# Optimization experiments

Measured on AMD Instinct MI355X. Metric: run time of the kernel, lower is better.

The kernel has to match this reference:

```python
import jax, jax.numpy as jnp
import numpy as np

B, OUT_LEN, IN_LEN, H = 8, 1024, 4096, 256


def setup_inputs() -> dict:
    key = jax.random.key(0)
    k1, k2, k3 = jax.random.split(key, 3)
    output = jax.random.normal(k1, (B, OUT_LEN, H), dtype=jnp.float32)
    encoder_outputs = jax.random.normal(k2, (B, IN_LEN, H), dtype=jnp.float32)
    # valid lengths in [1, IN_LEN] so every softmax row has >=1 unmasked entry
    lengths = jax.random.randint(k3, (B,), 1, IN_LEN + 1).astype(jnp.int32)
    return {"output": output, "encoder_outputs": encoder_outputs, "lengths": lengths}


def reference(output, encoder_outputs, lengths):
    # scores: [B, out_len, in_len], unscaled dot-product (as in the original)
    scores = jnp.einsum('boh,bih->boi', output, encoder_outputs)
    # mask[b, j] = j < lengths[b]; masked positions get -inf (additive mask)
    valid = jnp.arange(encoder_outputs.shape[1])[None, :] < lengths[:, None]  # [B, in_len]
    scores = jnp.where(valid[:, None, :], scores, -jnp.inf)
    attn = jax.nn.softmax(scores, axis=-1)  # [B, out_len, in_len]
    context = jnp.einsum('boi,bih->boh', attn, encoder_outputs)  # [B, out_len, H]
    return (context, attn)
```

## Files before the change

### kernel.cpp

```cpp
#include <hip/hip_runtime.h>
#include <hip/hip_bf16.h>
#include <math.h>

#define B_    8
#define OLEN  1024
#define ILEN  4096
#define HDIM  256
#define LDA   40

typedef __attribute__((ext_vector_type(8))) short bf16x8;
typedef __attribute__((ext_vector_type(4))) float f32x4;

__device__ inline unsigned pk_bf16(float x, float y) {
  union { __hip_bfloat162 h; unsigned u; } c;
  c.h = __float22bfloat162_rn(make_float2(x, y));
  return c.u;
}
__device__ inline short f2bf(float x) {
  union { __hip_bfloat16 h; short s; } c;
  c.h = __float2bfloat16(x);
  return c.s;
}

struct HiLo { uint4 hi, lo; };
__device__ inline HiLo split8(const float* __restrict__ p) {
  float4 v0 = *(const float4*)p;
  float4 v1 = *(const float4*)(p + 4);
  float f[8] = {v0.x, v0.y, v0.z, v0.w, v1.x, v1.y, v1.z, v1.w};
  unsigned hu[8]; float lo[8];
#pragma unroll
  for (int i = 0; i < 8; ++i) {
    unsigned u = __float_as_uint(f[i]);
    hu[i] = u & 0xffff0000u;
    lo[i] = f[i] - __uint_as_float(hu[i]);
  }
  HiLo r;
  r.hi = make_uint4((hu[0] >> 16) | hu[1], (hu[2] >> 16) | hu[3],
                    (hu[4] >> 16) | hu[5], (hu[6] >> 16) | hu[7]);
  r.lo = make_uint4(pk_bf16(lo[0], lo[1]), pk_bf16(lo[2], lo[3]),
                    pk_bf16(lo[4], lo[5]), pk_bf16(lo[6], lo[7]));
  return r;
}

__device__ inline void gl_lds16(const void* g, void* l) {
  __builtin_amdgcn_global_load_lds(
      (const __attribute__((address_space(1))) unsigned*)g,
      (__attribute__((address_space(3))) unsigned*)(l), 16, 0, 0);
}

__global__ __launch_bounds__(256) void k_prep_q(const float* __restrict__ Q,
                                                short* __restrict__ Qhi,
                                                short* __restrict__ Qlo) {
  const size_t idx = ((size_t)blockIdx.x * 256 + threadIdx.x) * 8;
  HiLo r = split8(&Q[idx]);
  *(uint4*)&Qhi[idx] = r.hi;
  *(uint4*)&Qlo[idx] = r.lo;
}

__global__ __launch_bounds__(256) void k_prep_e(const float* __restrict__ E,
                                                short* __restrict__ Ehi,
                                                short* __restrict__ Elo,
                                                short* __restrict__ ET,
                                                const int* __restrict__ len) {
  const int it = blockIdx.x, ht = blockIdx.y, b = blockIdx.z;
  const int L = len[b];
  const int t = threadIdx.x;
  if (it * 32 >= L) {
    const int h = t >> 3, i0 = (t & 7) * 4;
    *(uint2*)&ET[((size_t)(b * HDIM + ht * 32 + h)) * ILEN + it * 32 + i0] =
        make_uint2(0u, 0u);
    return;
  }
  __shared__ short Lsh[32][36];
  {
    const int i = t >> 3, h0 = (t & 7) * 4;
    const size_t gidx = ((size_t)(b * ILEN + it * 32 + i)) * HDIM + ht * 32 + h0;
    float4 v = *(const float4*)&E[gidx];
    float f[4] = {v.x, v.y, v.z, v.w};
    unsigned hs[4]; float lo[4];
#pragma unroll
    for (int j = 0; j < 4; ++j) {
      unsigned u = __float_as_uint(f[j]);
      hs[j] = u & 0xffff0000u;
      lo[j] = f[j] - __uint_as_float(hs[j]);
    }
    *(uint2*)&Ehi[gidx] = make_uint2((hs[0] >> 16) | hs[1], (hs[2] >> 16) | hs[3]);
    *(uint2*)&Elo[gidx] = make_uint2(pk_bf16(lo[0], lo[1]), pk_bf16(lo[2], lo[3]));
    Lsh[h0 + 0][i] = f2bf(f[0]);
    Lsh[h0 + 1][i] = f2bf(f[1]);
    Lsh[h0 + 2][i] = f2bf(f[2]);
    Lsh[h0 + 3][i] = f2bf(f[3]);
  }
  __syncthreads();
  {
    const int h = t >> 3, i0 = (t & 7) * 4;
    *(uint2*)&ET[((size_t)(b * HDIM + ht * 32 + h)) * ILEN + it * 32 + i0] =
        *(const uint2*)&Lsh[h][i0];
  }
}

__global__ __launch_bounds__(256) void k_scores_pre(
    const short* __restrict__ Qhi, const short* __restrict__ Qlo,
    const short* __restrict__ Ehi, const short* __restrict__ Elo,
    float* __restrict__ S, float2* __restrict__ stat,
    const int* __restrict__ len) {
  const int it = blockIdx.x, ot = blockIdx.y, b = blockIdx.z;
  const int L = len[b];
  if (it * 128 >= L) return;

  const size_t qoff = ((size_t)b * OLEN + ot * 128) * HDIM;
  const size_t eoff = ((size_t)b * ILEN + it * 128) * HDIM;

  __shared__ __align__(16) short Ah[128 * 32], Al[128 * 32];
  __shared__ __align__(16) short Bh[128 * 32], Bl[128 * 32];

  const int t = threadIdx.x;
  const int w = t >> 6, l = t & 63;
  const int la = l & 15, quad = l >> 4;
  const int mw = (w & 1) * 64, nw = (w >> 1) * 64;

  int sgoff[2], sloff[2];
#pragma unroll
  for (int j = 0; j < 2; ++j) {
    const int row = (w * 2 + j) * 16 + (l >> 2);
    const int c = (l & 3) ^ ((row >> 1) & 3);
    sgoff[j] = row * HDIM + c * 8;
    sloff[j] = ((w * 2 + j) * 64 + l) * 8;
  }

  f32x4 acc[4][4] = {};

  for (int kc = 0; kc < HDIM; kc += 32) {
#pragma unroll
    for (int j = 0; j < 2; ++j) {
      const size_t ga = qoff + sgoff[j] + kc;
      const size_t gb = eoff + sgoff[j] + kc;
      gl_lds16(&Qhi[ga], &Ah[sloff[j]]);
      gl_lds16(&Qlo[ga], &Al[sloff[j]]);
      gl_lds16(&Ehi[gb], &Bh[sloff[j]]);
      gl_lds16(&Elo[gb], &Bl[sloff[j]]);
    }
    __syncthreads();
    bf16x8 ah[4], al[4];
#pragma unroll
    for (int mi = 0; mi < 4; ++mi) {
      const int row = mw + mi * 16 + la;
      const int off = row * 32 + (quad ^ ((row >> 1) & 3)) * 8;
      ah[mi] = *(const bf16x8*)&Ah[off];
      al[mi] = *(const bf16x8*)&Al[off];
    }
#pragma unroll
    for (int ni = 0; ni < 4; ++ni) {
      const int row = nw + ni * 16 + la;
      const int off = row * 32 + (quad ^ ((row >> 1) & 3)) * 8;
      bf16x8 bh = *(const bf16x8*)&Bh[off];
      bf16x8 bl = *(const bf16x8*)&Bl[off];
#pragma unroll
      for (int mi = 0; mi < 4; ++mi) {
        acc[mi][ni] = __builtin_amdgcn_mfma_f32_16x16x32_bf16(ah[mi], bh, acc[mi][ni], 0, 0, 0);
        acc[mi][ni] = __builtin_amdgcn_mfma_f32_16x16x32_bf16(ah[mi], bl, acc[mi][ni], 0, 0, 0);
        acc[mi][ni] = __builtin_amdgcn_mfma_f32_16x16x32_bf16(al[mi], bh, acc[mi][ni], 0, 0, 0);
      }
    }
    __syncthreads();
  }

  float* Sb = S + ((size_t)b * OLEN + ot * 128) * (size_t)ILEN + it * 128;
#pragma unroll
  for (int mi = 0; mi < 4; ++mi)
#pragma unroll
    for (int ni = 0; ni < 4; ++ni)
#pragma unroll
      for (int r = 0; r < 4; ++r)
        Sb[(size_t)(mw + mi * 16 + quad * 4 + r) * ILEN + nw + ni * 16 + la] =
            acc[mi][ni][r];

  float* SM = (float*)Ah;
  float* SS = SM + 256;
  const int colbase = it * 128 + nw;

  float rmax[4][4];
#pragma unroll
  for (int mi = 0; mi < 4; ++mi)
#pragma unroll
    for (int r = 0; r < 4; ++r) {
      float mx = -INFINITY;
#pragma unroll
      for (int ni = 0; ni < 4; ++ni)
        if (colbase + ni * 16 + la < L) mx = fmaxf(mx, acc[mi][ni][r]);
      rmax[mi][r] = mx;
    }
#pragma unroll
  for (int o = 1; o < 16; o <<= 1)
#pragma unroll
    for (int mi = 0; mi < 4; ++mi)
#pragma unroll
      for (int r = 0; r < 4; ++r)
        rmax[mi][r] = fmaxf(rmax[mi][r], __shfl_xor(rmax[mi][r], o, 64));
  if (la == 0) {
#pragma unroll
    for (int mi = 0; mi < 4; ++mi)
#pragma unroll
      for (int r = 0; r < 4; ++r)
        SM[(w >> 1) * 128 + mw + mi * 16 + quad * 4 + r] = rmax[mi][r];
  }
  __syncthreads();

  float rsum[4][4];
#pragma unroll
  for (int mi = 0; mi < 4; ++mi)
#pragma unroll
    for (int r = 0; r < 4; ++r) {
      const int row = mw + mi * 16 + quad * 4 + r;
      const float M = fmaxf(SM[row], SM[128 + row]);
      float s = 0.f;
#pragma unroll
      for (int ni = 0; ni < 4; ++ni)
        if (colbase + ni * 16 + la < L) s += __expf(acc[mi][ni][r] - M);
      rsum[mi][r] = s;
    }
#pragma unroll
  for (int o = 1; o < 16; o <<= 1)
#pragma unroll
    for (int mi = 0; mi < 4; ++mi)
#pragma unroll
      for (int r = 0; r < 4; ++r)
        rsum[mi][r] += __shfl_xor(rsum[mi][r], o, 64);
  if (la == 0) {
#pragma unroll
    for (int mi = 0; mi < 4; ++mi)
#pragma unroll
      for (int r = 0; r < 4; ++r)
        SS[(w >> 1) * 128 + mw + mi * 16 + quad * 4 + r] = rsum[mi][r];
  }
  __syncthreads();

  if (t < 128) {
    const float m = fmaxf(SM[t], SM[128 + t]);
    const float s = SS[t] + SS[128 + t];
    stat[(size_t)it * (B_ * OLEN) + (size_t)b * OLEN + ot * 128 + t] =
        make_float2(m, s);
  }
}

__global__ __launch_bounds__(256) void k_combine(const float2* __restrict__ stat,
                                                 float2* __restrict__ rowstat,
                                                 const int* __restrict__ len) {
  const int row = blockIdx.x * 256 + threadIdx.x;
  const int b = row >> 10;
  const int L = len[b];
  const int nt = (L + 127) >> 7;
  float m = -INFINITY;
  for (int it = 0; it < nt; ++it)
    m = fmaxf(m, stat[(size_t)it * (B_ * OLEN) + row].x);
  float s = 0.f;
  for (int it = 0; it < nt; ++it) {
    float2 v = stat[(size_t)it * (B_ * OLEN) + row];
    s += v.y * __expf(v.x - m);
  }
  rowstat[row] = make_float2(m, 1.f / s);
}

__global__ __launch_bounds__(256) void k_context_fused(
    float* __restrict__ P, const short* __restrict__ ET,
    float* __restrict__ Cpart, const float2* __restrict__ rowstat,
    const int* __restrict__ len) {
  const int ot = blockIdx.x, ks = blockIdx.y, b = blockIdx.z;
  float* Pb = P + ((size_t)b * OLEN + ot * 64) * (size_t)ILEN + ks * 2048;
  const short* Tb = ET + (size_t)b * HDIM * ILEN + ks * 2048;
  const int L = len[b];

  __shared__ __align__(16) short As[64 * 64];
  __shared__ __align__(16) short Bs[256 * 64];

  const int t = threadIdx.x;
  const int w = t >> 6, l = t & 63;
  const int la = l & 15, quad = l >> 4;
  const int mw = (w & 1) * 32, nw = (w >> 1) * 128;

  const int tr = t >> 2, tc = t & 3;
  const int ac0 = tc * 2;
  const float2 st = rowstat[(size_t)b * OLEN + ot * 64 + tr];
  const float rm = st.x, rinv = st.y;

  int bslot[8];
#pragma unroll
  for (int j = 0; j < 8; ++j) bslot[j] = w * 512 + j * 64 + l;

  f32x4 acc[2][8] = {};

  for (int ic = 0; ic < 2048; ic += 64) {
    const int ibase = ks * 2048 + ic;
    float* arow = &Pb[(size_t)tr * ILEN + ic + tc * 16];
    if (ibase >= L) {
      const float4 z = make_float4(0.f, 0.f, 0.f, 0.f);
      *(float4*)(arow + 0) = z;
      *(float4*)(arow + 4) = z;
      *(float4*)(arow + 8) = z;
      *(float4*)(arow + 12) = z;
      continue;
    }
#pragma unroll
    for (int j = 0; j < 8; ++j) {
      const int s = bslot[j];
      const int row = s >> 3, pc = s & 7;
      const int c = pc ^ (row & 7);
      gl_lds16(&Tb[(size_t)row * ILEN + ic + c * 8], &Bs[s * 8]);
    }
    {
      float4 f0 = *(const float4*)(arow + 0);
      float4 f1 = *(const float4*)(arow + 4);
      float4 f2 = *(const float4*)(arow + 8);
      float4 f3 = *(const float4*)(arow + 12);
      float v[16] = {f0.x, f0.y, f0.z, f0.w, f1.x, f1.y, f1.z, f1.w,
                     f2.x, f2.y, f2.z, f2.w, f3.x, f3.y, f3.z, f3.w};
      const int i0 = ibase + tc * 16;
#pragma unroll
      for (int j = 0; j < 16; ++j)
        v[j] = (i0 + j < L) ? __expf(v[j] - rm) * rinv : 0.f;
      *(float4*)(arow + 0)  = make_float4(v[0], v[1], v[2], v[3]);
      *(float4*)(arow + 4)  = make_float4(v[4], v[5], v[6], v[7]);
      *(float4*)(arow + 8)  = make_float4(v[8], v[9], v[10], v[11]);
      *(float4*)(arow + 12) = make_float4(v[12], v[13], v[14], v[15]);
      uint4 w0 = make_uint4(pk_bf16(v[0], v[1]), pk_bf16(v[2], v[3]),
                            pk_bf16(v[4], v[5]), pk_bf16(v[6], v[7]));
      uint4 w1 = make_uint4(pk_bf16(v[8], v[9]), pk_bf16(v[10], v[11]),
                            pk_bf16(v[12], v[13]), pk_bf16(v[14], v[15]));
      *(uint4*)&As[tr * 64 + ((ac0) ^ (tr & 7)) * 8] = w0;
      *(uint4*)&As[tr * 64 + ((ac0 + 1) ^ (tr & 7)) * 8] = w1;
    }
    __syncthreads();
#pragma unroll
    for (int ki = 0; ki < 2; ++ki) {
      bf16x8 af[2];
#pragma unroll
      for (int mi = 0; mi < 2; ++mi) {
        const int row = mw + mi * 16 + la;
        af[mi] = *(const bf16x8*)&As[row * 64 + ((ki * 4 + quad) ^ (row & 7)) * 8];
      }
#pragma unroll
      for (int ni = 0; ni < 8; ++ni) {
        const int row = nw + ni * 16 + la;
        bf16x8 bfr = *(const bf16x8*)&Bs[row * 64 + ((ki * 4 + quad) ^ (row & 7)) * 8];
#pragma unroll
        for (int mi = 0; mi < 2; ++mi)
          acc[mi][ni] = __builtin_amdgcn_mfma_f32_16x16x32_bf16(af[mi], bfr,
                                                               acc[mi][ni], 0, 0, 0);
      }
    }
    __syncthreads();
  }

  float* Cb = Cpart + (size_t)ks * (B_ * OLEN * HDIM) +
              ((size_t)b * OLEN + ot * 64) * HDIM;
#pragma unroll
  for (int mi = 0; mi < 2; ++mi)
#pragma unroll
    for (int ni = 0; ni < 8; ++ni)
#pragma unroll
      for (int r = 0; r < 4; ++r)
        Cb[(size_t)(mw + mi * 16 + quad * 4 + r) * HDIM + nw + ni * 16 + la] =
            acc[mi][ni][r];
}

__global__ __launch_bounds__(256) void k_reduce(const float* __restrict__ Cp,
                                                float* __restrict__ ctx) {
  const size_t idx = ((size_t)blockIdx.x * 256 + threadIdx.x) * 8;
  const size_t n = (size_t)B_ * OLEN * HDIM;
  float4 a0 = *(const float4*)&Cp[idx];
  float4 a1 = *(const float4*)&Cp[idx + 4];
  float4 b0 = *(const float4*)&Cp[n + idx];
  float4 b1 = *(const float4*)&Cp[n + idx + 4];
  *(float4*)&ctx[idx] = make_float4(a0.x + b0.x, a0.y + b0.y, a0.z + b0.z, a0.w + b0.w);
  *(float4*)&ctx[idx + 4] = make_float4(a1.x + b1.x, a1.y + b1.y, a1.z + b1.z, a1.w + b1.w);
}

__global__ __launch_bounds__(256) void k_softmax(float* __restrict__ A,
                                                 const int* __restrict__ len) {
  const int row = blockIdx.x;
  const int b   = row >> 10;
  const int L   = len[b];
  float* p = A + (size_t)row * ILEN;
  const int t = threadIdx.x;

  float v[16];
#pragma unroll
  for (int k = 0; k < 4; ++k) {
    float4 x = *(const float4*)&p[4 * t + 1024 * k];
    v[4 * k + 0] = x.x; v[4 * k + 1] = x.y;
    v[4 * k + 2] = x.z; v[4 * k + 3] = x.w;
  }
  float m = -INFINITY;
#pragma unroll
  for (int k = 0; k < 4; ++k)
#pragma unroll
    for (int j = 0; j < 4; ++j) {
      const int i = 4 * t + 1024 * k + j;
      if (i < L) m = fmaxf(m, v[4 * k + j]);
    }
  for (int o = 32; o > 0; o >>= 1) m = fmaxf(m, __shfl_xor(m, o, 64));
  __shared__ float sm[4], ss[4];
  const int w = t >> 6;
  if ((t & 63) == 0) sm[w] = m;
  __syncthreads();
  m = fmaxf(fmaxf(sm[0], sm[1]), fmaxf(sm[2], sm[3]));
  float s = 0.f;
#pragma unroll
  for (int k = 0; k < 4; ++k)
#pragma unroll
    for (int j = 0; j < 4; ++j) {
      const int i = 4 * t + 1024 * k + j;
      float pv = (i < L) ? __expf(v[4 * k + j] - m) : 0.f;
      v[4 * k + j] = pv;
      s += pv;
    }
  for (int o = 32; o > 0; o >>= 1) s += __shfl_xor(s, o, 64);
  if ((t & 63) == 0) ss[w] = s;
  __syncthreads();
  s = ss[0] + ss[1] + ss[2] + ss[3];
  const float inv = 1.f / s;
#pragma unroll
  for (int k = 0; k < 4; ++k) {
    float4 x = make_float4(v[4 * k + 0] * inv, v[4 * k + 1] * inv,
                           v[4 * k + 2] * inv, v[4 * k + 3] * inv);
    *(float4*)&p[4 * t + 1024 * k] = x;
  }
}

__global__ __launch_bounds__(256) void k_etrans(const float* __restrict__ E,
                                                short* __restrict__ ET) {
  const int it = blockIdx.x, ht = blockIdx.y, b = blockIdx.z;
  __shared__ short Lsh[32][36];
  const int t = threadIdx.x;
  {
    const int i = t >> 3, h0 = (t & 7) * 4;
    float4 v = *(const float4*)&E[((size_t)(b * ILEN + it * 32 + i)) * HDIM + ht * 32 + h0];
    Lsh[h0 + 0][i] = f2bf(v.x);
    Lsh[h0 + 1][i] = f2bf(v.y);
    Lsh[h0 + 2][i] = f2bf(v.z);
    Lsh[h0 + 3][i] = f2bf(v.w);
  }
  __syncthreads();
  {
    const int h = t >> 3, i0 = (t & 7) * 4;
    *(uint2*)&ET[((size_t)(b * HDIM + ht * 32 + h)) * ILEN + it * 32 + i0] =
        *(const uint2*)&Lsh[h][i0];
  }
}

__global__ __launch_bounds__(256) void k_scores_split(const float* __restrict__ Q,
                                                      const float* __restrict__ E,
                                                      float* __restrict__ S) {
  const int b = blockIdx.z, ot = blockIdx.y, it = blockIdx.x;
  const float* Qb = Q + ((size_t)b * OLEN + ot * 64) * HDIM;
  const float* Eb = E + ((size_t)b * ILEN + it * 64) * HDIM;

  __shared__ __align__(16) short Ah[64 * LDA], Al[64 * LDA];
  __shared__ __align__(16) short Bh[64 * LDA], Bl[64 * LDA];

  const int t = threadIdx.x;
  const int w = t >> 6, l = t & 63;
  const int la = l & 15, quad = l >> 4;
  const int sr = t >> 2, sc = (t & 3) * 8;

  f32x4 acc[4] = {};

#pragma unroll
  for (int kc = 0; kc < HDIM; kc += 32) {
    HiLo qa = split8(&Qb[(size_t)sr * HDIM + kc + sc]);
    HiLo eb = split8(&Eb[(size_t)sr * HDIM + kc + sc]);
    *(uint4*)&Ah[sr * LDA + sc] = qa.hi;
    *(uint4*)&Al[sr * LDA + sc] = qa.lo;
    *(uint4*)&Bh[sr * LDA + sc] = eb.hi;
    *(uint4*)&Bl[sr * LDA + sc] = eb.lo;
    __syncthreads();
    bf16x8 ah = *(const bf16x8*)&Ah[(w * 16 + la) * LDA + quad * 8];
    bf16x8 al = *(const bf16x8*)&Al[(w * 16 + la) * LDA + quad * 8];
#pragma unroll
    for (int n = 0; n < 4; ++n) {
      bf16x8 bh = *(const bf16x8*)&Bh[(n * 16 + la) * LDA + quad * 8];
      bf16x8 bl = *(const bf16x8*)&Bl[(n * 16 + la) * LDA + quad * 8];
      acc[n] = __builtin_amdgcn_mfma_f32_16x16x32_bf16(ah, bh, acc[n], 0, 0, 0);
      acc[n] = __builtin_amdgcn_mfma_f32_16x16x32_bf16(ah, bl, acc[n], 0, 0, 0);
      acc[n] = __builtin_amdgcn_mfma_f32_16x16x32_bf16(al, bh, acc[n], 0, 0, 0);
    }
    __syncthreads();
  }

  float* Sb = S + ((size_t)b * OLEN + ot * 64) * (size_t)ILEN + it * 64;
#pragma unroll
  for (int n = 0; n < 4; ++n)
#pragma unroll
    for (int r = 0; r < 4; ++r)
      Sb[(size_t)(w * 16 + quad * 4 + r) * ILEN + n * 16 + la] = acc[n][r];
}

__global__ __launch_bounds__(256) void k_context_f32(const float* __restrict__ P,
                                                     const short* __restrict__ ET,
                                                     float* __restrict__ C) {
  const int ot = blockIdx.x, ht = blockIdx.y, b = blockIdx.z;
  const float* Pb = P + ((size_t)b * OLEN + ot * 64) * (size_t)ILEN;
  const short* Tb = ET + ((size_t)b * HDIM + ht * 64) * (size_t)ILEN;

  __shared__ __align__(16) short As[64 * LDA], Bs[64 * LDA];

  const int t = threadIdx.x;
  const int w = t >> 6, l = t & 63;
  const int la = l & 15, quad = l >> 4;
  const int sr = t >> 2, sc = (t & 3) * 8;

  f32x4 acc[4] = {};

  for (int ic = 0; ic < ILEN; ic += 32) {
    {
      float4 p0 = *(const float4*)&Pb[(size_t)sr * ILEN + ic + sc];
      float4 p1 = *(const float4*)&Pb[(size_t)sr * ILEN + ic + sc + 4];
      uint4 aw = make_uint4(pk_bf16(p0.x, p0.y), pk_bf16(p0.z, p0.w),
                            pk_bf16(p1.x, p1.y), pk_bf16(p1.z, p1.w));
      *(uint4*)&As[sr * LDA + sc] = aw;
      uint4 bw = *(const uint4*)&Tb[(size_t)sr * ILEN + ic + sc];
      *(uint4*)&Bs[sr * LDA + sc] = bw;
    }
    __syncthreads();
    bf16x8 a = *(const bf16x8*)&As[(w * 16 + la) * LDA + quad * 8];
#pragma unroll
    for (int n = 0; n < 4; ++n) {
      bf16x8 bb = *(const bf16x8*)&Bs[(n * 16 + la) * LDA + quad * 8];
      acc[n] = __builtin_amdgcn_mfma_f32_16x16x32_bf16(a, bb, acc[n], 0, 0, 0);
    }
    __syncthreads();
  }

  float* Cb = C + ((size_t)b * OLEN + ot * 64) * HDIM + ht * 64;
#pragma unroll
  for (int n = 0; n < 4; ++n)
#pragma unroll
    for (int r = 0; r < 4; ++r)
      Cb[(size_t)(w * 16 + quad * 4 + r) * HDIM + n * 16 + la] = acc[n][r];
}

extern "C" void kernel_launch(void* const* d_in, const int* in_sizes, int n_in,
                              void* d_out, int out_size, void* d_ws, size_t ws_size,
                              hipStream_t stream) {
  (void)in_sizes; (void)n_in; (void)out_size;
  const float* outp = (const float*)d_in[0];
  const float* enc  = (const float*)d_in[1];
  const int*   len  = (const int*)d_in[2];

  float* ctx  = (float*)d_out;
  float* attn = ctx + (size_t)B_ * OLEN * HDIM;

  short* ws = (short*)d_ws;
  const size_t M = 1024 * 1024;
  short* ET = ws;

  if (ws_size >= 56ull * 1024 * 1024) {
    short* Qhi = ws + 8 * M;
    short* Qlo = ws + 10 * M;
    short* Ehi = ws + 12 * M;
    short* Elo = ws + 20 * M;
    float* Cpart = (float*)(ws + 8 * M);
    float2* stat = (float2*)ctx;
    float2* rowstat = stat + (size_t)(ILEN / 128) * B_ * OLEN;

    k_prep_q<<<(B_ * OLEN * HDIM) / (256 * 8), 256, 0, stream>>>(outp, Qhi, Qlo);
    dim3 gp(ILEN / 32, HDIM / 32, B_);
    k_prep_e<<<gp, 256, 0, stream>>>(enc, Ehi, Elo, ET, len);
    dim3 g1(ILEN / 128, OLEN / 128, B_);
    k_scores_pre<<<g1, 256, 0, stream>>>(Qhi, Qlo, Ehi, Elo, attn, stat, len);
    k_combine<<<(B_ * OLEN) / 256, 256, 0, stream>>>(stat, rowstat, len);
    dim3 g3(OLEN / 64, 2, B_);
    k_context_fused<<<g3, 256, 0, stream>>>(attn, ET, Cpart, rowstat, len);
    k_reduce<<<(B_ * OLEN * HDIM) / (256 * 8), 256, 0, stream>>>(Cpart, ctx);
  } else {
    dim3 gt(ILEN / 32, HDIM / 32, B_);
    k_etrans<<<gt, 256, 0, stream>>>(enc, ET);
    k_scores_split<<<dim3(ILEN / 64, OLEN / 64, B_), 256, 0, stream>>>(outp, enc, attn);
    k_softmax<<<B_ * OLEN, 256, 0, stream>>>(attn, len);
    dim3 g3(OLEN / 64, HDIM / 64, B_);
    k_context_f32<<<g3, 256, 0, stream>>>(attn, ET, ctx);
  }
}
```

Measured before the change: 323.1 us.

## Split context GEMM four ways, prefetch next P tile, unroll combine loads

The fused context kernel now splits the input length four ways instead of two, doubling the grid to spread work across more compute units and balance the variable valid lengths. Zero-filling of masked tiles is hoisted into its own loop, and the next probability tile is loaded into registers while the current tile's MFMAs run. The reduce kernel sums four partials instead of two. The combine kernel issues all 32 stat loads up front with smaller blocks. The cost is more partial-sum traffic, more reduce work and higher register pressure.

```diff
diff --git a/kernel.cpp b/kernel.cpp
--- a/kernel.cpp
+++ b/kernel.cpp
@@ -7,6 +7,7 @@
 #define ILEN  4096
 #define HDIM  256
 #define LDA   40
+#define KSPLIT 4
 
 typedef __attribute__((ext_vector_type(8))) short bf16x8;
 typedef __attribute__((ext_vector_type(4))) float f32x4;
@@ -243,21 +244,24 @@
   }
 }
 
-__global__ __launch_bounds__(256) void k_combine(const float2* __restrict__ stat,
+__global__ __launch_bounds__(128) void k_combine(const float2* __restrict__ stat,
                                                  float2* __restrict__ rowstat,
                                                  const int* __restrict__ len) {
-  const int row = blockIdx.x * 256 + threadIdx.x;
+  const int row = blockIdx.x * 128 + threadIdx.x;
   const int b = row >> 10;
-  const int L = len[b];
-  const int nt = (L + 127) >> 7;
+  const int nt = (len[b] + 127) >> 7;
+  float2 v[32];
+#pragma unroll
+  for (int it = 0; it < 32; ++it)
+    v[it] = stat[(size_t)it * (B_ * OLEN) + row];
   float m = -INFINITY;
-  for (int it = 0; it < nt; ++it)
-    m = fmaxf(m, stat[(size_t)it * (B_ * OLEN) + row].x);
+#pragma unroll
+  for (int it = 0; it < 32; ++it)
+    if (it < nt) m = fmaxf(m, v[it].x);
   float s = 0.f;
-  for (int it = 0; it < nt; ++it) {
-    float2 v = stat[(size_t)it * (B_ * OLEN) + row];
-    s += v.y * __expf(v.x - m);
-  }
+#pragma unroll
+  for (int it = 0; it < 32; ++it)
+    if (it < nt) s += v[it].y * __expf(v[it].x - m);
   rowstat[row] = make_float2(m, 1.f / s);
 }
 
@@ -266,8 +270,9 @@
     float* __restrict__ Cpart, const float2* __restrict__ rowstat,
     const int* __restrict__ len) {
   const int ot = blockIdx.x, ks = blockIdx.y, b = blockIdx.z;
-  float* Pb = P + ((size_t)b * OLEN + ot * 64) * (size_t)ILEN + ks * 2048;
-  const short* Tb = ET + (size_t)b * HDIM * ILEN + ks * 2048;
+  const int NC = ILEN / KSPLIT;
+  float* Pb = P + ((size_t)b * OLEN + ot * 64) * (size_t)ILEN + ks * NC;
+  const short* Tb = ET + (size_t)b * HDIM * ILEN + ks * NC;
   const int L = len[b];
 
   __shared__ __align__(16) short As[64 * 64];
@@ -289,35 +294,44 @@
 
   f32x4 acc[2][8] = {};
 
-  for (int ic = 0; ic < 2048; ic += 64) {
-    const int ibase = ks * 2048 + ic;
+  const int rem = L - ks * NC;
+  const int nv = rem <= 0 ? 0 : (rem >= NC ? NC / 64 : (rem + 63) >> 6);
+
+  for (int ic = nv * 64; ic < NC; ic += 64) {
     float* arow = &Pb[(size_t)tr * ILEN + ic + tc * 16];
-    if (ibase >= L) {
-      const float4 z = make_float4(0.f, 0.f, 0.f, 0.f);
-      *(float4*)(arow + 0) = z;
-      *(float4*)(arow + 4) = z;
-      *(float4*)(arow + 8) = z;
-      *(float4*)(arow + 12) = z;
-      continue;
-    }
+    const float4 z = make_float4(0.f, 0.f, 0.f, 0.f);
+    *(float4*)(arow + 0)  = z;
+    *(float4*)(arow + 4)  = z;
+    *(float4*)(arow + 8)  = z;
+    *(float4*)(arow + 12) = z;
+  }
+
+  float4 f0, f1, f2, f3;
+  if (nv > 0) {
+    const float* src = &Pb[(size_t)tr * ILEN + tc * 16];
+    f0 = *(const float4*)(src + 0);
+    f1 = *(const float4*)(src + 4);
+    f2 = *(const float4*)(src + 8);
+    f3 = *(const float4*)(src + 12);
+  }
+
+  for (int c = 0; c < nv; ++c) {
+    const int ic = c * 64;
 #pragma unroll
     for (int j = 0; j < 8; ++j) {
       const int s = bslot[j];
       const int row = s >> 3, pc = s & 7;
-      const int c = pc ^ (row & 7);
-      gl_lds16(&Tb[(size_t)row * ILEN + ic + c * 8], &Bs[s * 8]);
+      const int cc = pc ^ (row & 7);
+      gl_lds16(&Tb[(size_t)row * ILEN + ic + cc * 8], &Bs[s * 8]);
     }
     {
-      float4 f0 = *(const float4*)(arow + 0);
-      float4 f1 = *(const float4*)(arow + 4);
-      float4 f2 = *(const float4*)(arow + 8);
-      float4 f3 = *(const float4*)(arow + 12);
       float v[16] = {f0.x, f0.y, f0.z, f0.w, f1.x, f1.y, f1.z, f1.w,
                      f2.x, f2.y, f2.z, f2.w, f3.x, f3.y, f3.z, f3.w};
-      const int i0 = ibase + tc * 16;
+      const int i0 = ks * NC + ic + tc * 16;
 #pragma unroll
       for (int j = 0; j < 16; ++j)
         v[j] = (i0 + j < L) ? __expf(v[j] - rm) * rinv : 0.f;
+      float* arow = &Pb[(size_t)tr * ILEN + ic + tc * 16];
       *(float4*)(arow + 0)  = make_float4(v[0], v[1], v[2], v[3]);
       *(float4*)(arow + 4)  = make_float4(v[4], v[5], v[6], v[7]);
       *(float4*)(arow + 8)  = make_float4(v[8], v[9], v[10], v[11]);
@@ -330,6 +344,13 @@
       *(uint4*)&As[tr * 64 + ((ac0 + 1) ^ (tr & 7)) * 8] = w1;
     }
     __syncthreads();
+    if (c + 1 < nv) {
+      const float* src = &Pb[(size_t)tr * ILEN + (c + 1) * 64 + tc * 16];
+      f0 = *(const float4*)(src + 0);
+      f1 = *(const float4*)(src + 4);
+      f2 = *(const float4*)(src + 8);
+      f3 = *(const float4*)(src + 12);
+    }
 #pragma unroll
     for (int ki = 0; ki < 2; ++ki) {
       bf16x8 af[2];
@@ -367,12 +388,22 @@
                                                 float* __restrict__ ctx) {
   const size_t idx = ((size_t)blockIdx.x * 256 + threadIdx.x) * 8;
   const size_t n = (size_t)B_ * OLEN * HDIM;
-  float4 a0 = *(const float4*)&Cp[idx];
-  float4 a1 = *(const float4*)&Cp[idx + 4];
-  float4 b0 = *(const float4*)&Cp[n + idx];
-  float4 b1 = *(const float4*)&Cp[n + idx + 4];
-  *(float4*)&ctx[idx] = make_float4(a0.x + b0.x, a0.y + b0.y, a0.z + b0.z, a0.w + b0.w);
-  *(float4*)&ctx[idx + 4] = make_float4(a1.x + b1.x, a1.y + b1.y, a1.z + b1.z, a1.w + b1.w);
+  float a[8];
+  {
+    float4 a0 = *(const float4*)&Cp[idx];
+    float4 a1 = *(const float4*)&Cp[idx + 4];
+    a[0] = a0.x; a[1] = a0.y; a[2] = a0.z; a[3] = a0.w;
+    a[4] = a1.x; a[5] = a1.y; a[6] = a1.z; a[7] = a1.w;
+  }
+#pragma unroll
+  for (int k = 1; k < KSPLIT; ++k) {
+    float4 b0 = *(const float4*)&Cp[(size_t)k * n + idx];
+    float4 b1 = *(const float4*)&Cp[(size_t)k * n + idx + 4];
+    a[0] += b0.x; a[1] += b0.y; a[2] += b0.z; a[3] += b0.w;
+    a[4] += b1.x; a[5] += b1.y; a[6] += b1.z; a[7] += b1.w;
+  }
+  *(float4*)&ctx[idx]     = make_float4(a[0], a[1], a[2], a[3]);
+  *(float4*)&ctx[idx + 4] = make_float4(a[4], a[5], a[6], a[7]);
 }
 
 __global__ __launch_bounds__(256) void k_softmax(float* __restrict__ A,
@@ -568,8 +599,8 @@
     k_prep_e<<<gp, 256, 0, stream>>>(enc, Ehi, Elo, ET, len);
     dim3 g1(ILEN / 128, OLEN / 128, B_);
     k_scores_pre<<<g1, 256, 0, stream>>>(Qhi, Qlo, Ehi, Elo, attn, stat, len);
-    k_combine<<<(B_ * OLEN) / 256, 256, 0, stream>>>(stat, rowstat, len);
-    dim3 g3(OLEN / 64, 2, B_);
+    k_combine<<<(B_ * OLEN) / 128, 128, 0, stream>>>(stat, rowstat, len);
+    dim3 g3(OLEN / 64, KSPLIT, B_);
     k_context_fused<<<g3, 256, 0, stream>>>(attn, ET, Cpart, rowstat, len);
     k_reduce<<<(B_ * OLEN * HDIM) / (256 * 8), 256, 0, stream>>>(Cpart, ctx);
   } else {
```

Result: slower. 355.2 us (+9.9%).
